# Kernel tuning notes

Hardware: AMD Instinct MI355X
Metric: run time of the kernel (lower is better)

Reference implementation:

```python
import jax, jax.numpy as jnp
import numpy as np

B, T, C = 4, 2048, 1024
H = 16
D = C // H  # head_dim = 64


def setup_inputs() -> dict:
    key = jax.random.key(0)
    k1, k2, k3, k4, k5 = jax.random.split(key, 5)
    s = 1.0 / np.sqrt(C)
    return {
        "hidden_state": jax.random.normal(k1, (B, T, C), dtype=jnp.float32),
        "qkv_w": jax.random.uniform(k2, (C, 3 * C), jnp.float32, -s, s),
        "qkv_b": jax.random.uniform(k3, (3 * C,), jnp.float32, -s, s),
        "o_w": jax.random.uniform(k4, (C, C), jnp.float32, -s, s),
        "o_b": jax.random.uniform(k5, (C,), jnp.float32, -s, s),
    }


def reference(hidden_state, qkv_w, qkv_b, o_w, o_b):
    Bq, Tq, Cq = hidden_state.shape
    qkv = hidden_state @ qkv_w + qkv_b  # [B,T,3C]
    q, k, v = jnp.split(qkv, 3, axis=-1)
    # [B,T,C] -> [B,H,T,D]
    q = q.reshape(Bq, Tq, H, D).transpose(0, 2, 1, 3)
    k = k.reshape(Bq, Tq, H, D).transpose(0, 2, 1, 3)
    v = v.reshape(Bq, Tq, H, D).transpose(0, 2, 1, 3)
    scaling = D ** (-0.5)
    scores = jnp.einsum("bhqd,bhkd->bhqk", q, k) * scaling  # [B,H,T,T]
    causal = jnp.tril(jnp.ones((Tq, Tq), dtype=bool))
    scores = jnp.where(causal[None, None], scores, -jnp.inf)
    attn = jax.nn.softmax(scores, axis=-1)
    out = jnp.einsum("bhqk,bhkd->bhqd", attn, v)  # [B,H,T,D]
    out = out.transpose(0, 2, 1, 3).reshape(Bq, Tq, Cq)
    return out @ o_w + o_b
```

## Files before the change

### kernel.cpp

```cpp
#include <hip/hip_runtime.h>
#include <hip/hip_bf16.h>

#define Bn 4
#define Tn 2048
#define Cn 1024
#define Hn 16
#define Dn 64
#define Kdim 1024

typedef __bf16 bf16x8 __attribute__((ext_vector_type(8)));
typedef float f32x4 __attribute__((ext_vector_type(4)));
union B8 { uint4 u; bf16x8 f; ushort s[8]; };

static __device__ __forceinline__ ushort f2bf(float x) {
    __hip_bfloat16 h = __float2bfloat16(x);
    return *(ushort*)&h;
}

#define AS1 __attribute__((address_space(1)))
#define AS3 __attribute__((address_space(3)))

static __device__ __forceinline__ void gload_lds16(const ushort* g, ushort* l) {
    __builtin_amdgcn_global_load_lds((AS1 const uint4*)(const void*)g,
                                     (AS3 uint4*)(void*)l, 16, 0, 0);
}

__global__ __launch_bounds__(256) void prep_fused(
    const float* __restrict__ X, const float* __restrict__ qkv_w,
    const float* __restrict__ o_w,
    ushort* __restrict__ Xb, ushort* __restrict__ Wqt, ushort* __restrict__ Wot)
{
    if (blockIdx.y == 0) {
        int i = (blockIdx.x * 256 + threadIdx.x) * 8;
        float4 a = *(const float4*)&X[i];
        float4 b = *(const float4*)&X[i + 4];
        ushort4 o0, o1;
        o0.x = f2bf(a.x); o0.y = f2bf(a.y); o0.z = f2bf(a.z); o0.w = f2bf(a.w);
        o1.x = f2bf(b.x); o1.y = f2bf(b.y); o1.z = f2bf(b.z); o1.w = f2bf(b.w);
        *(ushort4*)&Xb[i] = o0;
        *(ushort4*)&Xb[i + 4] = o1;
        return;
    }
    const float* W; ushort* Wt; int N, bx;
    if (blockIdx.y == 1) { W = qkv_w; Wt = Wqt; N = 3 * Cn; bx = blockIdx.x; }
    else                 { W = o_w;   Wt = Wot; N = Cn;     bx = blockIdx.x; }
    if (bx >= (N / 32) * 32) return;
    const int n0 = (bx % (N / 32)) * 32, k0 = (bx / (N / 32)) * 32;
    __shared__ float Ls[32][33];
    const int tx = threadIdx.x & 31, ty = threadIdx.x >> 5;
    #pragma unroll
    for (int i = 0; i < 4; i++) {
        int r = ty + i * 8;
        Ls[r][tx] = W[(size_t)(k0 + r) * N + n0 + tx];
    }
    __syncthreads();
    #pragma unroll
    for (int i = 0; i < 4; i++) {
        int r = ty + i * 8;
        Wt[(size_t)(n0 + r) * Kdim + k0 + tx] = f2bf(Ls[tx][r]);
    }
}

template <int EPI>
__global__ __launch_bounds__(256) void gemm_bt(
    const ushort* __restrict__ A, const ushort* __restrict__ Bt,
    const float* __restrict__ bias,
    float* __restrict__ Out, ushort* __restrict__ Qb,
    ushort* __restrict__ Kb, ushort* __restrict__ Vtb)
{
    const int nbx = gridDim.x;
    const int nwg = nbx * gridDim.y;
    const int bid = blockIdx.y * nbx + blockIdx.x;
    const int cpx = nwg >> 3;
    const int wg  = (bid & 7) * cpx + (bid >> 3);
    const int m0 = (wg / nbx) * 128;
    const int n0 = (wg % nbx) * 128;
    const int t  = threadIdx.x;
    const int wave = t >> 6, lane = t & 63;
    const int ln = lane & 15, quad = lane >> 4;
    const int wm = wave >> 1, wn = wave & 1;

    __shared__ ushort As[128 * 64];
    __shared__ ushort Bs[128 * 64];

    f32x4 acc[4][4] = {};

    for (int k0 = 0; k0 < Kdim; k0 += 64) {
        __syncthreads();
        #pragma unroll
        for (int it = 0; it < 4; it++) {
            int c = it * 256 + wave * 64 + lane;
            int row = c >> 3, seg = c & 7;
            int gseg = seg ^ (row & 7);
            gload_lds16(&A [(size_t)(m0 + row) * Kdim + k0 + gseg * 8], &As[c * 8]);
            gload_lds16(&Bt[(size_t)(n0 + row) * Kdim + k0 + gseg * 8], &Bs[c * 8]);
        }
        __syncthreads();

        #pragma unroll
        for (int ks = 0; ks < 2; ks++) {
            bf16x8 af[4], bf[4];
            #pragma unroll
            for (int mm = 0; mm < 4; mm++) {
                int row = wm * 64 + mm * 16 + ln;
                int seg = (ks * 4 + quad) ^ (ln & 7);
                B8 tmp; tmp.u = *(const uint4*)&As[row * 64 + seg * 8];
                af[mm] = tmp.f;
            }
            #pragma unroll
            for (int nn = 0; nn < 4; nn++) {
                int row = wn * 64 + nn * 16 + ln;
                int seg = (ks * 4 + quad) ^ (ln & 7);
                B8 tmp; tmp.u = *(const uint4*)&Bs[row * 64 + seg * 8];
                bf[nn] = tmp.f;
            }
            #pragma unroll
            for (int mm = 0; mm < 4; mm++)
                #pragma unroll
                for (int nn = 0; nn < 4; nn++)
                    acc[mm][nn] = __builtin_amdgcn_mfma_f32_16x16x32_bf16(
                        af[mm], bf[nn], acc[mm][nn], 0, 0, 0);
        }
    }

    if (EPI == 0) {
        #pragma unroll
        for (int nn = 0; nn < 4; nn++) {
            int n = n0 + wn * 64 + nn * 16 + ln;
            float bv = bias[n];
            #pragma unroll
            for (int mm = 0; mm < 4; mm++) {
                int mbase = m0 + wm * 64 + mm * 16 + quad * 4;
                #pragma unroll
                for (int reg = 0; reg < 4; reg++)
                    Out[(size_t)(mbase + reg) * 1024 + n] = acc[mm][nn][reg] + bv;
            }
        }
    } else {
        const int nb = n0 + wn * 64;
        const int which = nb >> 10;
        const int h = (nb & 1023) >> 6;
        const float scale = (which == 0) ? 0.125f * 1.44269504088896f : 1.0f;
        const int b_ = m0 >> 11;
        const int t0 = (m0 & 2047) + wm * 64;

        __syncthreads();
        ushort* tile = ((wave & 2) ? Bs : As) + (wave & 1) * 4096;

        if (which == 2) {
            #pragma unroll
            for (int nn = 0; nn < 4; nn++) {
                float bv = bias[nb + nn * 16 + ln];
                #pragma unroll
                for (int mm = 0; mm < 4; mm++)
                    #pragma unroll
                    for (int reg = 0; reg < 4; reg++) {
                        int m = mm * 16 + quad * 4 + reg;
                        int n = nn * 16 + ln;
                        tile[n * 64 + (m ^ (((n >> 1) & 7) * 8))] =
                            f2bf(acc[mm][nn][reg] + bv);
                    }
            }
            #pragma unroll
            for (int it = 0; it < 8; it++) {
                int idx = it * 64 + lane;
                int row = idx >> 3, seg = idx & 7;
                uint4 v = *(const uint4*)&tile[row * 64 +
                              ((seg * 8) ^ (((row >> 1) & 7) * 8))];
                *(uint4*)&Vtb[((size_t)((b_ * Hn + h) * Dn) + row) * Tn + t0 + seg * 8] = v;
            }
        } else {
            ushort* dst = (which == 0) ? Qb : Kb;
            #pragma unroll
            for (int nn = 0; nn < 4; nn++) {
                float bv = bias[nb + nn * 16 + ln];
                #pragma unroll
                for (int mm = 0; mm < 4; mm++)
                    #pragma unroll
                    for (int reg = 0; reg < 4; reg++) {
                        int m = mm * 16 + quad * 4 + reg;
                        int n = nn * 16 + ln;
                        tile[m * 64 + (n ^ (((m >> 1) & 7) * 8))] =
                            f2bf((acc[mm][nn][reg] + bv) * scale);
                    }
            }
            #pragma unroll
            for (int it = 0; it < 8; it++) {
                int idx = it * 64 + lane;
                int row = idx >> 3, seg = idx & 7;
                uint4 v = *(const uint4*)&tile[row * 64 +
                              ((seg * 8) ^ (((row >> 1) & 7) * 8))];
                *(uint4*)&dst[((size_t)((b_ * Hn + h) * Tn) + t0 + row) * Dn + seg * 8] = v;
            }
        }
    }
}

__global__ __launch_bounds__(256, 2) void attn_mfma(
    const ushort* __restrict__ Qb, const ushort* __restrict__ Kb,
    const ushort* __restrict__ Vtb, ushort* __restrict__ Ob)
{
    const int bh   = blockIdx.x;
    const int yp   = blockIdx.y;
    const int t    = threadIdx.x;
    const int wave = t >> 6, lane = t & 63;
    const int ln   = lane & 15, quad = lane >> 4;

    __shared__ ushort Ks[2][128 * 64];
    __shared__ ushort Ps[4][2][4][16 * 34];

    const ushort* KgB = Kb  + (size_t)bh * Tn * Dn;
    const ushort* VgB = Vtb + (size_t)bh * Dn * Tn;
    const int b_ = bh >> 4, h = bh & 15;

    B8 ones;
    #pragma unroll
    for (int j = 0; j < 8; j++) ones.s[j] = 0x3F80;

    #define STAGE_K(kc, buf)                                                   \
        do {                                                                   \
            _Pragma("unroll")                                                  \
            for (int it = 0; it < 4; it++) {                                   \
                int c = it * 256 + wave * 64 + lane;                           \
                int row = c >> 3, seg = c & 7;                                 \
                int gs = seg ^ (row & 7);                                      \
                gload_lds16(&KgB[(size_t)((kc) * 128 + row) * Dn + gs * 8],    \
                            &Ks[buf][c * 8]);                                  \
            }                                                                  \
        } while (0)

    for (int pass = 0; pass < 2; pass++) {
        const int qt = pass ? yp : 15 - yp;
        if (pass) __syncthreads();

        int cur = 0;
        STAGE_K(0, 0);

        const int q0 = qt * 128;
        const ushort* Qg = Qb + ((size_t)bh * Tn + q0 + wave * 32) * Dn;
        bf16x8 qf[2][2];
        #pragma unroll
        for (int ns = 0; ns < 2; ns++)
            #pragma unroll
            for (int ks = 0; ks < 2; ks++) {
                B8 tmp; tmp.u = *(const uint4*)&Qg[(ns * 16 + ln) * 64 + ks * 32 + quad * 8];
                qf[ns][ks] = tmp.f;
            }

        f32x4 Oacc[4][2] = {};
        f32x4 Lacc[2] = {};
        float m_r[2] = {0.f, 0.f};

        for (int kc = 0; kc <= qt; kc++) {
            __syncthreads();

            B8 vfr[4][4];
            #pragma unroll
            for (int gks = 0; gks < 4; gks++)
                #pragma unroll
                for (int ctd = 0; ctd < 4; ctd++)
                    vfr[ctd][gks].u = *(const uint4*)&VgB[
                        (size_t)(ctd * 16 + ln) * Tn + kc * 128 + gks * 32 + quad * 8];

            if (kc < qt) STAGE_K(kc + 1, cur ^ 1);

            const ushort* Kc = Ks[cur];
            f32x4 S[8][2] = {};
            #pragma unroll
            for (int ks = 0; ks < 2; ks++)
                #pragma unroll
                for (int ct = 0; ct < 8; ct++) {
                    B8 a; a.u = *(const uint4*)&Kc[(ct * 16 + ln) * 64 +
                                                   (((ks * 4 + quad) ^ (ln & 7)) * 8)];
                    #pragma unroll
                    for (int ns = 0; ns < 2; ns++)
                        S[ct][ns] = __builtin_amdgcn_mfma_f32_16x16x32_bf16(
                            a.f, qf[ns][ks], S[ct][ns], 0, 0, 0);
                }

            if (kc == qt) {
                #pragma unroll
                for (int ct = 0; ct < 8; ct++) {
                    int keyl = ct * 16 + quad * 4;
                    #pragma unroll
                    for (int ns = 0; ns < 2; ns++) {
                        int ql = wave * 32 + ns * 16 + ln;
                        #pragma unroll
                        for (int reg = 0; reg < 4; reg++)
                            if (keyl + reg > ql) S[ct][ns][reg] = -1e30f;
                    }
                }
            }

            float pm[2], m_old[2];
            #pragma unroll
            for (int ns = 0; ns < 2; ns++) {
                m_old[ns] = m_r[ns];
                float ctm[8];
                #pragma unroll
                for (int ct = 0; ct < 8; ct++)
                    ctm[ct] = fmaxf(fmaxf(S[ct][ns][0], S[ct][ns][1]),
                                    fmaxf(S[ct][ns][2], S[ct][ns][3]));
                float p = fmaxf(fmaxf(fmaxf(ctm[0], ctm[1]), fmaxf(ctm[2], ctm[3])),
                                fmaxf(fmaxf(ctm[4], ctm[5]), fmaxf(ctm[6], ctm[7])));
                p = fmaxf(p, __shfl_xor(p, 16));
                p = fmaxf(p, __shfl_xor(p, 32));
                pm[ns] = p;
            }

            #pragma unroll
            for (int ns = 0; ns < 2; ns++)
                #pragma unroll
                for (int ct = 0; ct < 8; ct++)
                    #pragma unroll
                    for (int reg = 0; reg < 4; reg++)
                        S[ct][ns][reg] = exp2f(S[ct][ns][reg] - m_old[ns]);

            bool need = (pm[0] > m_old[0] + 8.0f) | (pm[1] > m_old[1] + 8.0f);
            if (__any(need)) {
                #pragma unroll
                for (int ns = 0; ns < 2; ns++) {
                    float mn = fmaxf(m_old[ns], pm[ns]);
                    float alpha = exp2f(m_old[ns] - mn);
                    m_r[ns] = mn;
                    #pragma unroll
                    for (int ct = 0; ct < 8; ct++)
                        #pragma unroll
                        for (int reg = 0; reg < 4; reg++)
                            S[ct][ns][reg] *= alpha;
                    #pragma unroll
                    for (int ctd = 0; ctd < 4; ctd++)
                        Oacc[ctd][ns] *= alpha;
                    Lacc[ns] *= alpha;
                }
            }

            #pragma unroll
            for (int ns = 0; ns < 2; ns++)
                #pragma unroll
                for (int ct = 0; ct < 8; ct++) {
                    float s0 = S[ct][ns][0], s1 = S[ct][ns][1];
                    float s2 = S[ct][ns][2], s3 = S[ct][ns][3];
                    uint w0, w1;
                    asm("v_cvt_pk_bf16_f32 %0, %1, %2" : "=v"(w0) : "v"(s0), "v"(s1));
                    asm("v_cvt_pk_bf16_f32 %0, %1, %2" : "=v"(w1) : "v"(s2), "v"(s3));
                    uint2 o; o.x = w0; o.y = w1;
                    *(uint2*)&Ps[wave][ns][ct >> 1]
                        [ln * 34 + (ct & 1) * 16 + quad * 4] = o;
                }

            #pragma unroll
            for (int p = 0; p < 4; p++)
                #pragma unroll
                for (int ns = 0; ns < 2; ns++) {
                    B8 pfr; pfr.u = *(const uint4*)&Ps[wave][ns][p]
                        [ln * 34 + quad * 8];
                    #pragma unroll
                    for (int ctd = 0; ctd < 4; ctd++)
                        Oacc[ctd][ns] = __builtin_amdgcn_mfma_f32_16x16x32_bf16(
                            vfr[ctd][p].f, pfr.f, Oacc[ctd][ns], 0, 0, 0);
                    Lacc[ns] = __builtin_amdgcn_mfma_f32_16x16x32_bf16(
                        ones.f, pfr.f, Lacc[ns], 0, 0, 0);
                }
            cur ^= 1;
        }

        #pragma unroll
        for (int ns = 0; ns < 2; ns++) {
            float inv = 1.0f / Lacc[ns][0];
            int token = q0 + wave * 32 + ns * 16 + ln;
            ushort* dst = Ob + ((size_t)(b_ * Tn + token)) * Cn + h * 64;
            #pragma unroll
            for (int ctd = 0; ctd < 4; ctd++) {
                ushort4 o;
                #pragma unroll
                for (int reg = 0; reg < 4; reg++)
                    ((ushort*)&o)[reg] = f2bf(Oacc[ctd][ns][reg] * inv);
                *(ushort4*)&dst[ctd * 16 + quad * 4] = o;
            }
        }
    }
    #undef STAGE_K
}

extern "C" void kernel_launch(void* const* d_in, const int* in_sizes, int n_in,
                              void* d_out, int out_size, void* d_ws, size_t ws_size,
                              hipStream_t stream) {
    const float* X     = (const float*)d_in[0];
    const float* qkv_w = (const float*)d_in[1];
    const float* qkv_b = (const float*)d_in[2];
    const float* o_w   = (const float*)d_in[3];
    const float* o_b   = (const float*)d_in[4];
    float* out = (float*)d_out;

    const size_t BTC = (size_t)Bn * Tn * Cn;
    ushort* Xb  = (ushort*)d_ws;
    ushort* Wqt = Xb  + BTC;
    ushort* Wot = Wqt + 3 * Cn * Cn;
    ushort* Qb  = Wot + Cn * Cn;
    ushort* Kb  = Qb  + BTC;
    ushort* Vtb = Kb  + BTC;
    ushort* Ao  = Vtb + BTC;

    prep_fused<<<dim3(4096, 3), 256, 0, stream>>>(X, qkv_w, o_w, Xb, Wqt, Wot);

    gemm_bt<1><<<dim3(3 * Cn / 128, 8192 / 128), 256, 0, stream>>>(
        Xb, Wqt, qkv_b, nullptr, Qb, Kb, Vtb);
    attn_mfma<<<dim3(Bn * Hn, 8), 256, 0, stream>>>(Qb, Kb, Vtb, Ao);
    gemm_bt<0><<<dim3(Cn / 128, 8192 / 128), 256, 0, stream>>>(
        Ao, Wot, o_b, out, nullptr, nullptr, nullptr);
}
```

Before: 269.8 us.

## Stage V tiles through LDS with async loads and split P into halves

V fragments were loaded straight from global memory into 64 VGPRs per thread each iteration. They are now staged into a swizzled LDS tile with global_load_lds, issued alongside the K prefetch, and read back per PV sub-pass. The P buffer is halved: the softmax output is packed and consumed in two rounds of two 32-key slices. This cuts register pressure and makes the V loads coalesced, at the cost of an extra __syncthreads per iteration, more LDS traffic and a larger LDS footprint that could limit occupancy.

```diff
diff --git a/kernel.cpp b/kernel.cpp
--- a/kernel.cpp
+++ b/kernel.cpp
@@ -207,7 +207,8 @@
     const int ln   = lane & 15, quad = lane >> 4;
 
     __shared__ ushort Ks[2][128 * 64];
-    __shared__ ushort Ps[4][2][4][16 * 34];
+    __shared__ ushort Vs[64 * 128];
+    __shared__ ushort Ps[4][2][2][16 * 34];
 
     const ushort* KgB = Kb  + (size_t)bh * Tn * Dn;
     const ushort* VgB = Vtb + (size_t)bh * Dn * Tn;
@@ -229,6 +230,58 @@
             }                                                                  \
         } while (0)
 
+    #define STAGE_V(kc)                                                        \
+        do {                                                                   \
+            _Pragma("unroll")                                                  \
+            for (int it = 0; it < 4; it++) {                                   \
+                int c = it * 256 + wave * 64 + lane;                           \
+                int row = c >> 4, seg = c & 15;                                \
+                int gs = seg ^ (row & 7);                                      \
+                gload_lds16(&VgB[(size_t)row * Tn + (kc) * 128 + gs * 8],      \
+                            &Vs[c * 8]);                                       \
+            }                                                                  \
+        } while (0)
+
+    #define PACK_WRITE(p, pp)                                                  \
+        do {                                                                   \
+            _Pragma("unroll")                                                  \
+            for (int ns = 0; ns < 2; ns++)                                     \
+                _Pragma("unroll")                                              \
+                for (int cth = 0; cth < 2; cth++) {                            \
+                    int ct = (p) * 2 + cth;                                    \
+                    float s0 = S[ct][ns][0], s1 = S[ct][ns][1];                \
+                    float s2 = S[ct][ns][2], s3 = S[ct][ns][3];                \
+                    uint w0, w1;                                               \
+                    asm("v_cvt_pk_bf16_f32 %0, %1, %2"                         \
+                        : "=v"(w0) : "v"(s0), "v"(s1));                        \
+                    asm("v_cvt_pk_bf16_f32 %0, %1, %2"                         \
+                        : "=v"(w1) : "v"(s2), "v"(s3));                        \
+                    uint2 o; o.x = w0; o.y = w1;                               \
+                    *(uint2*)&Ps[wave][pp][ns]                                 \
+                        [ln * 34 + cth * 16 + quad * 4] = o;                   \
+                }                                                              \
+        } while (0)
+
+    #define PV_PASS(p, pp)                                                     \
+        do {                                                                   \
+            B8 vfrp[4];                                                        \
+            _Pragma("unroll")                                                  \
+            for (int ctd = 0; ctd < 4; ctd++)                                  \
+                vfrp[ctd].u = *(const uint4*)&Vs[(ctd * 16 + ln) * 128 +       \
+                    ((((p) * 4 + quad) ^ (ln & 7)) * 8)];                      \
+            _Pragma("unroll")                                                  \
+            for (int ns = 0; ns < 2; ns++) {                                   \
+                B8 pfr; pfr.u = *(const uint4*)&Ps[wave][pp][ns]               \
+                    [ln * 34 + quad * 8];                                      \
+                _Pragma("unroll")                                              \
+                for (int ctd = 0; ctd < 4; ctd++)                              \
+                    Oacc[ctd][ns] = __builtin_amdgcn_mfma_f32_16x16x32_bf16(   \
+                        vfrp[ctd].f, pfr.f, Oacc[ctd][ns], 0, 0, 0);           \
+                Lacc[ns] = __builtin_amdgcn_mfma_f32_16x16x32_bf16(            \
+                    ones.f, pfr.f, Lacc[ns], 0, 0, 0);                         \
+            }                                                                  \
+        } while (0)
+
     for (int pass = 0; pass < 2; pass++) {
         const int qt = pass ? yp : 15 - yp;
         if (pass) __syncthreads();
@@ -254,14 +307,7 @@
         for (int kc = 0; kc <= qt; kc++) {
             __syncthreads();
 
-            B8 vfr[4][4];
-            #pragma unroll
-            for (int gks = 0; gks < 4; gks++)
-                #pragma unroll
-                for (int ctd = 0; ctd < 4; ctd++)
-                    vfr[ctd][gks].u = *(const uint4*)&VgB[
-                        (size_t)(ctd * 16 + ln) * Tn + kc * 128 + gks * 32 + quad * 8];
-
+            STAGE_V(kc);
             if (kc < qt) STAGE_K(kc + 1, cur ^ 1);
 
             const ushort* Kc = Ks[cur];
@@ -335,33 +381,16 @@
                 }
             }
 
-            #pragma unroll
-            for (int ns = 0; ns < 2; ns++)
-                #pragma unroll
-                for (int ct = 0; ct < 8; ct++) {
-                    float s0 = S[ct][ns][0], s1 = S[ct][ns][1];
-                    float s2 = S[ct][ns][2], s3 = S[ct][ns][3];
-                    uint w0, w1;
-                    asm("v_cvt_pk_bf16_f32 %0, %1, %2" : "=v"(w0) : "v"(s0), "v"(s1));
-                    asm("v_cvt_pk_bf16_f32 %0, %1, %2" : "=v"(w1) : "v"(s2), "v"(s3));
-                    uint2 o; o.x = w0; o.y = w1;
-                    *(uint2*)&Ps[wave][ns][ct >> 1]
-                        [ln * 34 + (ct & 1) * 16 + quad * 4] = o;
-                }
-
-            #pragma unroll
-            for (int p = 0; p < 4; p++)
-                #pragma unroll
-                for (int ns = 0; ns < 2; ns++) {
-                    B8 pfr; pfr.u = *(const uint4*)&Ps[wave][ns][p]
-                        [ln * 34 + quad * 8];
-                    #pragma unroll
-                    for (int ctd = 0; ctd < 4; ctd++)
-                        Oacc[ctd][ns] = __builtin_amdgcn_mfma_f32_16x16x32_bf16(
-                            vfr[ctd][p].f, pfr.f, Oacc[ctd][ns], 0, 0, 0);
-                    Lacc[ns] = __builtin_amdgcn_mfma_f32_16x16x32_bf16(
-                        ones.f, pfr.f, Lacc[ns], 0, 0, 0);
-                }
+            PACK_WRITE(0, 0);
+            PACK_WRITE(1, 1);
+            __syncthreads();
+
+            PV_PASS(0, 0);
+            PV_PASS(1, 1);
+            PACK_WRITE(2, 0);
+            PACK_WRITE(3, 1);
+            PV_PASS(2, 0);
+            PV_PASS(3, 1);
             cur ^= 1;
         }
 
@@ -381,6 +410,9 @@
         }
     }
     #undef STAGE_K
+    #undef STAGE_V
+    #undef PACK_WRITE
+    #undef PV_PASS
 }
 
 extern "C" void kernel_launch(void* const* d_in, const int* in_sizes, int n_in,
```

Result: no change. 264.6 us (-1.9%).
